# Kernel optimization log

Hardware: AMD Instinct MI355X
Metric: run time of the kernel (lower is better)

The kernel has to match this reference:

```python
import jax, jax.numpy as jnp
import numpy as np

D_MODEL = 1024
D_STATE = 16
D_CONV = 4
EXPAND = 2
D_INNER = EXPAND * D_MODEL          # 2048
DT_RANK = D_INNER // 16             # 128
BATCH = 2
SEQLEN = 1024


def _silu(x):
    return x * jax.nn.sigmoid(x)


def setup_inputs() -> dict:
    key = jax.random.key(0)
    ks = jax.random.split(key, 8)
    s = 0.02
    A_init = jnp.tile(jnp.arange(1, D_STATE + 1, dtype=jnp.float32)[None, :], (D_INNER, 1))
    return {
        "x": jax.random.normal(ks[0], (BATCH, SEQLEN, D_MODEL), jnp.float32),
        "W_in": jax.random.normal(ks[1], (D_MODEL, 2 * D_INNER), jnp.float32) * s,
        "conv_k": jax.random.normal(ks[2], (D_CONV, 1, D_INNER), jnp.float32) * s,  # (kw, in/groups, out)
        "conv_b": jnp.zeros((D_INNER,), jnp.float32),
        "W_xproj": jax.random.normal(ks[3], (D_INNER, DT_RANK + 2 * D_STATE), jnp.float32) * s,
        "W_dt": jax.random.normal(ks[4], (DT_RANK, D_INNER), jnp.float32) * s,
        "b_dt": jnp.zeros((D_INNER,), jnp.float32),
        "A_log": jnp.log(A_init),
        "D": jnp.ones((D_INNER,), jnp.float32),
        "W_out": jax.random.normal(ks[5], (D_INNER, D_MODEL), jnp.float32) * s,
    }


def reference(x, W_in, conv_k, conv_b, W_xproj, W_dt, b_dt, A_log, D, W_out):
    # in_proj and gate split
    xz = x @ W_in                                   # (B, L, 2*Di)
    x_in, z = jnp.split(xz, 2, axis=-1)             # each (B, L, Di)

    # depthwise causal conv1d: left-pad by d_conv-1 (keras padding='causal')
    xp = jnp.pad(x_in, ((0, 0), (D_CONV - 1, 0), (0, 0)))
    x_in = jax.lax.conv_general_dilated(
        xp, conv_k, window_strides=(1,), padding='VALID',
        dimension_numbers=('NWC', 'WIO', 'NWC'),
        feature_group_count=D_INNER) + conv_b
    u = _silu(x_in)                                 # (B, L, Di)

    # input-dependent SSM params
    x_dbl = u @ W_xproj                             # (B, L, dt_rank + 2*N)
    dt_low, Bm, Cm = jnp.split(x_dbl, [DT_RANK, DT_RANK + D_STATE], axis=-1)
    dt = jax.nn.softplus(dt_low @ W_dt + b_dt)      # (B, L, Di)
    A = -jnp.exp(A_log)                             # (Di, N)
    dA = jnp.exp(jnp.einsum('bld,dn->bldn', dt, A)) # (B, L, Di, N)
    dB = jnp.einsum('bld,bln->bldn', dt, Bm)        # (B, L, Di, N)

    # selective scan over sequence length
    def step(h, e):
        a_t, b_t, u_t, c_t = e                      # (B,Di,N), (B,Di,N), (B,Di), (B,N)
        h = a_t * h + b_t * u_t[..., None]
        y_t = jnp.einsum('bdn,bn->bd', h, c_t)
        return h, y_t

    h0 = jnp.zeros((x.shape[0], D_INNER, D_STATE), dtype=x.dtype)
    xs = (jnp.swapaxes(dA, 0, 1), jnp.swapaxes(dB, 0, 1),
          jnp.swapaxes(u, 0, 1), jnp.swapaxes(Cm, 0, 1))
    _, yT = jax.lax.scan(step, h0, xs)              # (L, B, Di)
    y = jnp.swapaxes(yT, 0, 1) + u * D              # skip connection

    return (y * _silu(z)) @ W_out                   # (B, L, d_model)
```

## Files before the change

kernel.cpp:

```cpp
#include <hip/hip_runtime.h>
#include <hip/hip_bf16.h>

#define D_MODEL 1024
#define D_STATE 16
#define D_CONV 4
#define D_INNER 2048
#define DT_RANK 128
#define BATCH 2
#define SEQLEN 1024
#define XCOLS 160
#define NCHUNK 64
#define LCHUNK 16

typedef __hip_bfloat16 bf16;
typedef __attribute__((ext_vector_type(8))) short short8;
typedef __attribute__((ext_vector_type(4))) float f32x4;

__device__ __forceinline__ unsigned short f2bf_bits(float f) {
    bf16 h = __float2bfloat16(f);
    return *(unsigned short*)&h;
}
__device__ __forceinline__ float bfbits_to_f(unsigned int us) {
    return __uint_as_float(us << 16);
}

__device__ __forceinline__ float softplus_f(float x) {
    return fmaxf(x, 0.f) + __logf(1.f + __expf(-fabsf(x)));
}

__device__ __forceinline__ void load16_lds(void* lds, const void* g) {
    __builtin_amdgcn_global_load_lds(
        (const __attribute__((address_space(1))) unsigned int*)g,
        (__attribute__((address_space(3))) unsigned int*)lds, 16, 0, 0);
}

__device__ __forceinline__ void transpose_tile(const float* __restrict__ B,
                                               bf16* __restrict__ Bt,
                                               int K, int N, int nt, int kt,
                                               float (*t)[33], int tid)
{
    const int tx = tid & 31, ty = tid >> 5;
    const int n0 = nt * 32, k0 = kt * 32;
    #pragma unroll
    for (int r = 0; r < 4; ++r) {
        int n = n0 + tx;
        t[ty + r * 8][tx] = (n < N) ? B[(size_t)(k0 + ty + r * 8) * N + n] : 0.f;
    }
    __syncthreads();
    #pragma unroll
    for (int r = 0; r < 4; ++r)
        Bt[(size_t)(n0 + ty + r * 8) * K + k0 + tx] = __float2bfloat16(t[tx][ty + r * 8]);
}

__global__ __launch_bounds__(256)
void prep_kernel(const float* __restrict__ x, bf16* __restrict__ x_bf,
                 const float* __restrict__ W_in, bf16* __restrict__ Win_t,
                 const float* __restrict__ W_xproj, bf16* __restrict__ Wxp_t,
                 const float* __restrict__ W_dt, bf16* __restrict__ Wdt_t,
                 const float* __restrict__ W_out, bf16* __restrict__ Wout_t,
                 const float* __restrict__ A_log, float* __restrict__ Aneg)
{
    __shared__ float t[32][33];
    const int tid = threadIdx.x;
    int blk = blockIdx.x;
    if (blk < 4096) {
        transpose_tile(W_in, Win_t, D_MODEL, 2 * D_INNER, blk & 127, blk >> 7, t, tid);
        return;
    }
    blk -= 4096;
    if (blk < 512) {
        transpose_tile(W_xproj, Wxp_t, D_INNER, XCOLS, blk & 7, blk >> 3, t, tid);
        return;
    }
    blk -= 512;
    if (blk < 256) {
        transpose_tile(W_dt, Wdt_t, DT_RANK, D_INNER, blk & 63, blk >> 6, t, tid);
        return;
    }
    blk -= 256;
    if (blk < 2048) {
        transpose_tile(W_out, Wout_t, D_INNER, D_MODEL, blk & 31, blk >> 5, t, tid);
        return;
    }
    blk -= 2048;
    if (blk < 2048) {
        int i = blk * 256 + tid;
        float4 v = ((const float4*)x)[i];
        ushort4 p;
        p.x = f2bf_bits(v.x); p.y = f2bf_bits(v.y);
        p.z = f2bf_bits(v.z); p.w = f2bf_bits(v.w);
        ((ushort4*)x_bf)[i] = p;
        return;
    }
    blk -= 2048;
    {
        int i = blk * 256 + tid;
        Aneg[i] = -__expf(A_log[i]);
    }
}

template<int BN, int EPI>
__global__ __launch_bounds__(256)
void gemm_mfma(const bf16* __restrict__ A, const bf16* __restrict__ Bt,
               float* __restrict__ C, bf16* __restrict__ Cb,
               const float* __restrict__ bias,
               int M, int N, int K, int ldc, int kchunk)
{
    constexpr int WN = (BN == 128) ? 64 : 32;
    constexpr int NJ = WN / 16;
    __shared__ short As[128 * 32];
    __shared__ short Bs[BN * 32];
    const int tid = threadIdx.x;
    const int lane = tid & 63, wave = tid >> 6;
    const int wm = (wave >> 1) * 64, wn = (wave & 1) * WN;
    const int row0 = blockIdx.y * 128, col0 = blockIdx.x * BN;
    const int r_m = lane & 15, r_q = lane >> 4;
    const int kstart = blockIdx.z * kchunk;
    float* Cz = (EPI == 3) ? C : C + (size_t)blockIdx.z * M * ldc;

    const int srow = tid >> 2, schk = (tid & 3) * 8;
    const bf16* Ag0 = A  + (size_t)(row0 + srow)      * K + kstart + schk;
    const bf16* Ag1 = A  + (size_t)(row0 + srow + 64) * K + kstart + schk;
    const bf16* Bg0 = Bt + (size_t)(col0 + srow)      * K + kstart + schk;
    const bf16* Bg1 = Bt + (size_t)(col0 + srow + 64) * K + kstart + schk;
    short* AsW0 = &As[8 * tid];
    short* AsW1 = &As[8 * tid + 2048];
    short* BsW0 = &Bs[8 * tid];
    short* BsW1 = &Bs[8 * tid + 2048];

    f32x4 acc[4][NJ];
    #pragma unroll
    for (int i = 0; i < 4; ++i)
        #pragma unroll
        for (int j = 0; j < NJ; ++j)
            #pragma unroll
            for (int r = 0; r < 4; ++r) acc[i][j][r] = 0.f;

    for (int k0 = 0; k0 < kchunk; k0 += 32) {
        __syncthreads();
        load16_lds(AsW0, Ag0 + k0);
        load16_lds(AsW1, Ag1 + k0);
        load16_lds(BsW0, Bg0 + k0);
        if (BN == 128) load16_lds(BsW1, Bg1 + k0);
        __syncthreads();
        short8 af[4], bfr[NJ];
        #pragma unroll
        for (int i = 0; i < 4; ++i)
            af[i] = *(const short8*)&As[(wm + i * 16 + r_m) * 32 + r_q * 8];
        #pragma unroll
        for (int j = 0; j < NJ; ++j)
            bfr[j] = *(const short8*)&Bs[(wn + j * 16 + r_m) * 32 + r_q * 8];
        #pragma unroll
        for (int i = 0; i < 4; ++i)
            #pragma unroll
            for (int j = 0; j < NJ; ++j)
                acc[i][j] = __builtin_amdgcn_mfma_f32_16x16x32_bf16(
                    af[i], bfr[j], acc[i][j], 0, 0, 0);
    }

    #pragma unroll
    for (int i = 0; i < 4; ++i) {
        #pragma unroll
        for (int j = 0; j < NJ; ++j) {
            int row = row0 + wm + i * 16 + r_q * 4;
            int col = col0 + wn + j * 16 + r_m;
            if (col < N) {
                if (EPI == 1) {
                    float bv = bias[col];
                    #pragma unroll
                    for (int r = 0; r < 4; ++r)
                        Cb[(size_t)(row + r) * ldc + col] =
                            __float2bfloat16(softplus_f(acc[i][j][r] + bv));
                } else if (EPI == 2) {
                    if (col < D_INNER) {
                        #pragma unroll
                        for (int r = 0; r < 4; ++r)
                            Cz[(size_t)(row + r) * D_INNER + col] = acc[i][j][r];
                    } else {
                        #pragma unroll
                        for (int r = 0; r < 4; ++r)
                            Cb[(size_t)(row + r) * D_INNER + (col - D_INNER)] =
                                __float2bfloat16(acc[i][j][r]);
                    }
                } else if (EPI == 3) {
                    #pragma unroll
                    for (int r = 0; r < 4; ++r)
                        atomicAdd(&Cz[(size_t)(row + r) * ldc + col], acc[i][j][r]);
                } else {
                    #pragma unroll
                    for (int r = 0; r < 4; ++r)
                        Cz[(size_t)(row + r) * ldc + col] = acc[i][j][r];
                }
            }
        }
    }
}

__global__ __launch_bounds__(256)
void reduce_xdbl(const float* __restrict__ Cpart, float* __restrict__ x_dbl,
                 bf16* __restrict__ dtA_bf)
{
    int i = blockIdx.x * 256 + threadIdx.x;
    if (i >= 2048 * XCOLS) return;
    int r = i / XCOLS, c = i - r * XCOLS;
    float s = 0.f;
    #pragma unroll
    for (int z = 0; z < 8; ++z)
        s += Cpart[(size_t)z * 2048 * 256 + (size_t)r * 256 + c];
    x_dbl[i] = s;
    if (c < DT_RANK) dtA_bf[(size_t)r * DT_RANK + c] = __float2bfloat16(s);
}

__global__ __launch_bounds__(256)
void conv_silu_kernel(const float* __restrict__ xz32,
                      const float* __restrict__ conv_k,
                      const float* __restrict__ conv_b,
                      bf16* __restrict__ u_bf)
{
    int idx4 = blockIdx.x * 256 + threadIdx.x;
    int d4 = idx4 & (D_INNER / 4 - 1);
    int t = (idx4 >> 9) & (SEQLEN - 1);
    int b = idx4 >> 19;
    float4 acc = ((const float4*)conv_b)[d4];
    #pragma unroll
    for (int k = 0; k < D_CONV; ++k) {
        int tt = t + k - (D_CONV - 1);
        if (tt >= 0) {
            float4 xv = ((const float4*)xz32)[(size_t)(b * SEQLEN + tt) * (D_INNER / 4) + d4];
            float4 kv = ((const float4*)conv_k)[k * (D_INNER / 4) + d4];
            acc.x = fmaf(xv.x, kv.x, acc.x);
            acc.y = fmaf(xv.y, kv.y, acc.y);
            acc.z = fmaf(xv.z, kv.z, acc.z);
            acc.w = fmaf(xv.w, kv.w, acc.w);
        }
    }
    ushort4 pk;
    pk.x = f2bf_bits(acc.x / (1.f + __expf(-acc.x)));
    pk.y = f2bf_bits(acc.y / (1.f + __expf(-acc.y)));
    pk.z = f2bf_bits(acc.z / (1.f + __expf(-acc.z)));
    pk.w = f2bf_bits(acc.w / (1.f + __expf(-acc.w)));
    ((ushort4*)u_bf)[idx4] = pk;
}

__global__ __launch_bounds__(256)
void scan_phase1(const bf16* __restrict__ dt_sb,
                 const float* __restrict__ Aneg,
                 const bf16* __restrict__ u_bf,
                 const float* __restrict__ x_dbl,
                 unsigned int* __restrict__ PSp)
{
    __shared__ float Bsm[LCHUNK][16];
    const int d = blockIdx.x * 256 + threadIdx.x;
    const int c = blockIdx.y, b = blockIdx.z;
    const int t0 = c * LCHUNK;
    {
        int tt = threadIdx.x >> 4, n = threadIdx.x & 15;
        Bsm[tt][n] = x_dbl[(size_t)(b * SEQLEN + t0 + tt) * XCOLS + DT_RANK + n];
    }
    float A_row[D_STATE];
    {
        const float4* a4 = (const float4*)(Aneg + d * D_STATE);
        #pragma unroll
        for (int q = 0; q < 4; ++q) {
            float4 v = a4[q];
            A_row[q*4+0]=v.x; A_row[q*4+1]=v.y; A_row[q*4+2]=v.z; A_row[q*4+3]=v.w;
        }
    }
    __syncthreads();
    float P[D_STATE], S[D_STATE];
    #pragma unroll
    for (int n = 0; n < D_STATE; ++n) { P[n] = 1.f; S[n] = 0.f; }
    const bf16* dpp = dt_sb + (size_t)(b * SEQLEN + t0) * D_INNER + d;
    const bf16* upp = u_bf + (size_t)(b * SEQLEN + t0) * D_INNER + d;
    #pragma unroll
    for (int t = 0; t < LCHUNK; ++t) {
        float dtv = __bfloat162float(dpp[(size_t)t * D_INNER]);
        float du = dtv * __bfloat162float(upp[(size_t)t * D_INNER]);
        const float4* b4 = (const float4*)&Bsm[t][0];
        #pragma unroll
        for (int q = 0; q < 4; ++q) {
            float4 v = b4[q];
            float Bn[4] = {v.x, v.y, v.z, v.w};
            #pragma unroll
            for (int e = 0; e < 4; ++e) {
                int n = q * 4 + e;
                float a = __expf(dtv * A_row[n]);
                P[n] *= a;
                S[n] = fmaf(a, S[n], du * Bn[e]);
            }
        }
    }
    const size_t base = ((size_t)(b * NCHUNK + c) * D_STATE) * D_INNER + d;
    #pragma unroll
    for (int n = 0; n < D_STATE; ++n)
        PSp[base + (size_t)n * D_INNER] =
            ((unsigned int)f2bf_bits(S[n]) << 16) | f2bf_bits(P[n]);
}

__global__ __launch_bounds__(256)
void scan_phase2(const unsigned int* __restrict__ PSp, bf16* __restrict__ Hin)
{
    const int d = blockIdx.x * 256 + threadIdx.x;
    const int n = blockIdx.y;
    const int b = blockIdx.z;
    float h = 0.f;
    #pragma unroll 8
    for (int c = 0; c < NCHUNK; ++c) {
        const size_t idx = ((size_t)(b * NCHUNK + c) * D_STATE + n) * D_INNER + d;
        unsigned int ps = PSp[idx];
        float Pv = bfbits_to_f(ps & 0xffffu);
        float Sv = bfbits_to_f(ps >> 16);
        Hin[idx] = __float2bfloat16(h);
        h = fmaf(Pv, h, Sv);
    }
}

__global__ __launch_bounds__(256)
void scan_phase3(const bf16* __restrict__ dt_sb,
                 const float* __restrict__ Aneg,
                 const bf16* __restrict__ u_bf,
                 const float* __restrict__ x_dbl,
                 const float* __restrict__ Dvec,
                 const bf16* __restrict__ z_bf,
                 const bf16* __restrict__ Hin,
                 bf16* __restrict__ g_bf)
{
    __shared__ float BCs[LCHUNK][32];
    const int d = blockIdx.x * 256 + threadIdx.x;
    const int c = blockIdx.y, b = blockIdx.z;
    const int t0 = c * LCHUNK;
    {
        int i0 = threadIdx.x;
        int tt = i0 >> 5, col = i0 & 31;
        BCs[tt][col] = x_dbl[(size_t)(b * SEQLEN + t0 + tt) * XCOLS + DT_RANK + col];
        int i1 = i0 + 256;
        tt = i1 >> 5; col = i1 & 31;
        BCs[tt][col] = x_dbl[(size_t)(b * SEQLEN + t0 + tt) * XCOLS + DT_RANK + col];
    }
    float A_row[D_STATE];
    {
        const float4* a4 = (const float4*)(Aneg + d * D_STATE);
        #pragma unroll
        for (int q = 0; q < 4; ++q) {
            float4 v = a4[q];
            A_row[q*4+0]=v.x; A_row[q*4+1]=v.y; A_row[q*4+2]=v.z; A_row[q*4+3]=v.w;
        }
    }
    const float Dd = Dvec[d];
    __syncthreads();
    float h[D_STATE];
    const size_t base = ((size_t)(b * NCHUNK + c) * D_STATE) * D_INNER + d;
    #pragma unroll
    for (int n = 0; n < D_STATE; ++n)
        h[n] = __bfloat162float(Hin[base + (size_t)n * D_INNER]);
    const bf16* dpp = dt_sb + (size_t)(b * SEQLEN + t0) * D_INNER + d;
    const bf16* upp = u_bf + (size_t)(b * SEQLEN + t0) * D_INNER + d;
    const bf16* zpp = z_bf + (size_t)(b * SEQLEN + t0) * D_INNER + d;
    bf16* gpp = g_bf + (size_t)(b * SEQLEN + t0) * D_INNER + d;
    #pragma unroll
    for (int t = 0; t < LCHUNK; ++t) {
        float dtv = __bfloat162float(dpp[(size_t)t * D_INNER]);
        float uv = __bfloat162float(upp[(size_t)t * D_INNER]);
        float du = dtv * uv;
        float y = 0.f;
        const float4* bc4 = (const float4*)&BCs[t][0];
        #pragma unroll
        for (int q = 0; q < 4; ++q) {
            float4 v = bc4[q];
            float4 w = bc4[q + 4];
            float Bn[4] = {v.x, v.y, v.z, v.w};
            float Cn[4] = {w.x, w.y, w.z, w.w};
            #pragma unroll
            for (int e = 0; e < 4; ++e) {
                int n = q * 4 + e;
                float a = __expf(dtv * A_row[n]);
                h[n] = fmaf(a, h[n], du * Bn[e]);
                y = fmaf(h[n], Cn[e], y);
            }
        }
        float zv = __bfloat162float(zpp[(size_t)t * D_INNER]);
        float gy = y + uv * Dd;
        float sz = zv / (1.f + __expf(-zv));
        gpp[(size_t)t * D_INNER] = __float2bfloat16(gy * sz);
    }
}

extern "C" void kernel_launch(void* const* d_in, const int* in_sizes, int n_in,
                              void* d_out, int out_size, void* d_ws, size_t ws_size,
                              hipStream_t stream)
{
    const float* x      = (const float*)d_in[0];
    const float* W_in   = (const float*)d_in[1];
    const float* conv_k = (const float*)d_in[2];
    const float* conv_b = (const float*)d_in[3];
    const float* W_xproj= (const float*)d_in[4];
    const float* W_dt   = (const float*)d_in[5];
    const float* b_dt   = (const float*)d_in[6];
    const float* A_log  = (const float*)d_in[7];
    const float* Dvec   = (const float*)d_in[8];
    const float* W_out  = (const float*)d_in[9];
    float* out = (float*)d_out;

    const int BL = BATCH * SEQLEN;
    const size_t PS_ELEMS = (size_t)BATCH * NCHUNK * D_STATE * D_INNER;

    float* ws     = (float*)d_ws;
    float* xz32   = ws;
    float* x_dbl  = xz32   + (size_t)BL * D_INNER;
    float* Cpart3 = x_dbl  + (size_t)BL * XCOLS;
    unsigned int* PSp = (unsigned int*)(Cpart3 + 4194304);
    bf16* Hin     = (bf16*)(PSp + PS_ELEMS);
    float* Aneg   = (float*)(Hin + PS_ELEMS);
    bf16*  x_bf   = (bf16*)Cpart3;
    bf16* Win_t  = (bf16*)(Aneg + 32768);
    bf16* u_bf   = Win_t + (size_t)4096 * 1024;
    bf16* Wxp_t  = u_bf  + (size_t)BL * D_INNER;
    bf16* dtA_bf = Wxp_t + (size_t)256 * 2048;
    bf16* Wdt_t  = dtA_bf+ (size_t)BL * DT_RANK;
    bf16* g_bf   = Wdt_t + (size_t)2048 * 128;
    bf16* Wout_t = g_bf  + (size_t)BL * D_INNER;
    bf16* dt_sb  = Wout_t+ (size_t)1024 * 2048;
    bf16* z_bf   = dt_sb + (size_t)BL * D_INNER;

    hipMemsetAsync(out, 0, (size_t)out_size * sizeof(float), stream);
    prep_kernel<<<4096 + 512 + 256 + 2048 + 2048 + 128, 256, 0, stream>>>(
        x, x_bf, W_in, Win_t, W_xproj, Wxp_t, W_dt, Wdt_t, W_out, Wout_t, A_log, Aneg);

    gemm_mfma<128, 2><<<dim3(32, 16, 1), 256, 0, stream>>>(
        x_bf, Win_t, xz32, z_bf, nullptr, BL, 2 * D_INNER, D_MODEL, D_INNER, D_MODEL);

    conv_silu_kernel<<<(BL * D_INNER / 4) / 256, 256, 0, stream>>>(xz32, conv_k, conv_b, u_bf);

    gemm_mfma<64, 0><<<dim3(4, 16, 8), 256, 0, stream>>>(
        u_bf, Wxp_t, Cpart3, nullptr, nullptr, BL, 256, D_INNER, 256, 256);
    reduce_xdbl<<<(BL * XCOLS + 255) / 256, 256, 0, stream>>>(Cpart3, x_dbl, dtA_bf);

    gemm_mfma<64, 1><<<dim3(32, 16, 1), 256, 0, stream>>>(
        dtA_bf, Wdt_t, nullptr, dt_sb, b_dt, BL, D_INNER, DT_RANK, D_INNER, DT_RANK);

    scan_phase1<<<dim3(D_INNER / 256, NCHUNK, BATCH), 256, 0, stream>>>(
        dt_sb, Aneg, u_bf, x_dbl, PSp);
    scan_phase2<<<dim3(D_INNER / 256, D_STATE, BATCH), 256, 0, stream>>>(PSp, Hin);
    scan_phase3<<<dim3(D_INNER / 256, NCHUNK, BATCH), 256, 0, stream>>>(
        dt_sb, Aneg, u_bf, x_dbl, Dvec, z_bf, Hin, g_bf);

    gemm_mfma<64, 3><<<dim3(16, 16, 2), 256, 0, stream>>>(
        g_bf, Wout_t, out, nullptr, nullptr, BL, D_MODEL, D_INNER, D_MODEL, D_MODEL);
}
```

Before: 238.2 us.

## Prescale A by log2e for exp2, fold output zeroing into prep, reuse conv window

Scales A by log2(e) in the prep kernel so the scan phases can call exp2f directly and skip the multiply inside __expf. Replaces the separate hipMemsetAsync of the output with extra zeroing blocks in prep_kernel, removing one operation from the stream. Rewrites conv_silu so each thread produces four consecutive timesteps from a 7-row sliding window, cutting redundant loads of xz32 and conv weights. In exchange the conv kernel launches four times fewer threads and each thread does more work.

```diff
diff --git a/kernel.cpp b/kernel.cpp
--- a/kernel.cpp
+++ b/kernel.cpp
@@ -52,13 +52,16 @@
         Bt[(size_t)(n0 + ty + r * 8) * K + k0 + tx] = __float2bfloat16(t[tx][ty + r * 8]);
 }
 
+#define LOG2E 1.4426950408889634f
+
 __global__ __launch_bounds__(256)
 void prep_kernel(const float* __restrict__ x, bf16* __restrict__ x_bf,
                  const float* __restrict__ W_in, bf16* __restrict__ Win_t,
                  const float* __restrict__ W_xproj, bf16* __restrict__ Wxp_t,
                  const float* __restrict__ W_dt, bf16* __restrict__ Wdt_t,
                  const float* __restrict__ W_out, bf16* __restrict__ Wout_t,
-                 const float* __restrict__ A_log, float* __restrict__ Aneg)
+                 const float* __restrict__ A_log, float* __restrict__ A2,
+                 float* __restrict__ out_zero)
 {
     __shared__ float t[32][33];
     const int tid = threadIdx.x;
@@ -93,9 +96,16 @@
         return;
     }
     blk -= 2048;
+    if (blk < 128) {
+        int i = blk * 256 + tid;
+        A2[i] = -__expf(A_log[i]) * LOG2E;
+        return;
+    }
+    blk -= 128;
     {
         int i = blk * 256 + tid;
-        Aneg[i] = -__expf(A_log[i]);
+        float4 z = {0.f, 0.f, 0.f, 0.f};
+        ((float4*)out_zero)[i] = z;
     }
 }
 
@@ -217,34 +227,48 @@
                       const float* __restrict__ conv_b,
                       bf16* __restrict__ u_bf)
 {
-    int idx4 = blockIdx.x * 256 + threadIdx.x;
-    int d4 = idx4 & (D_INNER / 4 - 1);
-    int t = (idx4 >> 9) & (SEQLEN - 1);
-    int b = idx4 >> 19;
-    float4 acc = ((const float4*)conv_b)[d4];
-    #pragma unroll
-    for (int k = 0; k < D_CONV; ++k) {
-        int tt = t + k - (D_CONV - 1);
-        if (tt >= 0) {
-            float4 xv = ((const float4*)xz32)[(size_t)(b * SEQLEN + tt) * (D_INNER / 4) + d4];
-            float4 kv = ((const float4*)conv_k)[k * (D_INNER / 4) + d4];
-            acc.x = fmaf(xv.x, kv.x, acc.x);
-            acc.y = fmaf(xv.y, kv.y, acc.y);
-            acc.z = fmaf(xv.z, kv.z, acc.z);
-            acc.w = fmaf(xv.w, kv.w, acc.w);
-        }
-    }
-    ushort4 pk;
-    pk.x = f2bf_bits(acc.x / (1.f + __expf(-acc.x)));
-    pk.y = f2bf_bits(acc.y / (1.f + __expf(-acc.y)));
-    pk.z = f2bf_bits(acc.z / (1.f + __expf(-acc.z)));
-    pk.w = f2bf_bits(acc.w / (1.f + __expf(-acc.w)));
-    ((ushort4*)u_bf)[idx4] = pk;
+    int idx = blockIdx.x * 256 + threadIdx.x;
+    int d4 = idx & (D_INNER / 4 - 1);
+    int t4 = (idx >> 9) & (SEQLEN / 4 - 1);
+    int b  = idx >> 17;
+    const int t0 = t4 * 4;
+    float4 kv[D_CONV];
+    #pragma unroll
+    for (int k = 0; k < D_CONV; ++k)
+        kv[k] = ((const float4*)conv_k)[k * (D_INNER / 4) + d4];
+    const float4 bias = ((const float4*)conv_b)[d4];
+    float4 xv[7];
+    #pragma unroll
+    for (int j = 0; j < 7; ++j) {
+        int tt = t0 - 3 + j;
+        if (tt >= 0)
+            xv[j] = ((const float4*)xz32)[(size_t)(b * SEQLEN + tt) * (D_INNER / 4) + d4];
+        else
+            xv[j] = make_float4(0.f, 0.f, 0.f, 0.f);
+    }
+    #pragma unroll
+    for (int i = 0; i < 4; ++i) {
+        float4 acc = bias;
+        #pragma unroll
+        for (int k = 0; k < D_CONV; ++k) {
+            float4 xvk = xv[i + k];
+            acc.x = fmaf(xvk.x, kv[k].x, acc.x);
+            acc.y = fmaf(xvk.y, kv[k].y, acc.y);
+            acc.z = fmaf(xvk.z, kv[k].z, acc.z);
+            acc.w = fmaf(xvk.w, kv[k].w, acc.w);
+        }
+        ushort4 pk;
+        pk.x = f2bf_bits(acc.x / (1.f + __expf(-acc.x)));
+        pk.y = f2bf_bits(acc.y / (1.f + __expf(-acc.y)));
+        pk.z = f2bf_bits(acc.z / (1.f + __expf(-acc.z)));
+        pk.w = f2bf_bits(acc.w / (1.f + __expf(-acc.w)));
+        ((ushort4*)u_bf)[(size_t)(b * SEQLEN + t0 + i) * (D_INNER / 4) + d4] = pk;
+    }
 }
 
 __global__ __launch_bounds__(256)
 void scan_phase1(const bf16* __restrict__ dt_sb,
-                 const float* __restrict__ Aneg,
+                 const float* __restrict__ A2,
                  const bf16* __restrict__ u_bf,
                  const float* __restrict__ x_dbl,
                  unsigned int* __restrict__ PSp)
@@ -259,7 +283,7 @@
     }
     float A_row[D_STATE];
     {
-        const float4* a4 = (const float4*)(Aneg + d * D_STATE);
+        const float4* a4 = (const float4*)(A2 + d * D_STATE);
         #pragma unroll
         for (int q = 0; q < 4; ++q) {
             float4 v = a4[q];
@@ -284,7 +308,7 @@
             #pragma unroll
             for (int e = 0; e < 4; ++e) {
                 int n = q * 4 + e;
-                float a = __expf(dtv * A_row[n]);
+                float a = exp2f(dtv * A_row[n]);
                 P[n] *= a;
                 S[n] = fmaf(a, S[n], du * Bn[e]);
             }
@@ -317,7 +341,7 @@
 
 __global__ __launch_bounds__(256)
 void scan_phase3(const bf16* __restrict__ dt_sb,
-                 const float* __restrict__ Aneg,
+                 const float* __restrict__ A2,
                  const bf16* __restrict__ u_bf,
                  const float* __restrict__ x_dbl,
                  const float* __restrict__ Dvec,
@@ -339,7 +363,7 @@
     }
     float A_row[D_STATE];
     {
-        const float4* a4 = (const float4*)(Aneg + d * D_STATE);
+        const float4* a4 = (const float4*)(A2 + d * D_STATE);
         #pragma unroll
         for (int q = 0; q < 4; ++q) {
             float4 v = a4[q];
@@ -373,7 +397,7 @@
             #pragma unroll
             for (int e = 0; e < 4; ++e) {
                 int n = q * 4 + e;
-                float a = __expf(dtv * A_row[n]);
+                float a = exp2f(dtv * A_row[n]);
                 h[n] = fmaf(a, h[n], du * Bn[e]);
                 y = fmaf(h[n], Cn[e], y);
             }
@@ -410,9 +434,9 @@
     float* Cpart3 = x_dbl  + (size_t)BL * XCOLS;
     unsigned int* PSp = (unsigned int*)(Cpart3 + 4194304);
     bf16* Hin     = (bf16*)(PSp + PS_ELEMS);
-    float* Aneg   = (float*)(Hin + PS_ELEMS);
+    float* A2v    = (float*)(Hin + PS_ELEMS);
     bf16*  x_bf   = (bf16*)Cpart3;
-    bf16* Win_t  = (bf16*)(Aneg + 32768);
+    bf16* Win_t  = (bf16*)(A2v + 32768);
     bf16* u_bf   = Win_t + (size_t)4096 * 1024;
     bf16* Wxp_t  = u_bf  + (size_t)BL * D_INNER;
     bf16* dtA_bf = Wxp_t + (size_t)256 * 2048;
@@ -422,14 +446,15 @@
     bf16* dt_sb  = Wout_t+ (size_t)1024 * 2048;
     bf16* z_bf   = dt_sb + (size_t)BL * D_INNER;
 
-    hipMemsetAsync(out, 0, (size_t)out_size * sizeof(float), stream);
-    prep_kernel<<<4096 + 512 + 256 + 2048 + 2048 + 128, 256, 0, stream>>>(
-        x, x_bf, W_in, Win_t, W_xproj, Wxp_t, W_dt, Wdt_t, W_out, Wout_t, A_log, Aneg);
+    prep_kernel<<<4096 + 512 + 256 + 2048 + 2048 + 128 + 2048, 256, 0, stream>>>(
+        x, x_bf, W_in, Win_t, W_xproj, Wxp_t, W_dt, Wdt_t, W_out, Wout_t,
+        A_log, A2v, out);
 
     gemm_mfma<128, 2><<<dim3(32, 16, 1), 256, 0, stream>>>(
         x_bf, Win_t, xz32, z_bf, nullptr, BL, 2 * D_INNER, D_MODEL, D_INNER, D_MODEL);
 
-    conv_silu_kernel<<<(BL * D_INNER / 4) / 256, 256, 0, stream>>>(xz32, conv_k, conv_b, u_bf);
+    conv_silu_kernel<<<(BL * D_INNER / 16) / 256, 256, 0, stream>>>(
+        xz32, conv_k, conv_b, u_bf);
 
     gemm_mfma<64, 0><<<dim3(4, 16, 8), 256, 0, stream>>>(
         u_bf, Wxp_t, Cpart3, nullptr, nullptr, BL, 256, D_INNER, 256, 256);
@@ -439,10 +464,10 @@
         dtA_bf, Wdt_t, nullptr, dt_sb, b_dt, BL, D_INNER, DT_RANK, D_INNER, DT_RANK);
 
     scan_phase1<<<dim3(D_INNER / 256, NCHUNK, BATCH), 256, 0, stream>>>(
-        dt_sb, Aneg, u_bf, x_dbl, PSp);
+        dt_sb, A2v, u_bf, x_dbl, PSp);
     scan_phase2<<<dim3(D_INNER / 256, D_STATE, BATCH), 256, 0, stream>>>(PSp, Hin);
     scan_phase3<<<dim3(D_INNER / 256, NCHUNK, BATCH), 256, 0, stream>>>(
-        dt_sb, Aneg, u_bf, x_dbl, Dvec, z_bf, Hin, g_bf);
+        dt_sb, A2v, u_bf, x_dbl, Dvec, z_bf, Hin, g_bf);
 
     gemm_mfma<64, 3><<<dim3(16, 16, 2), 256, 0, stream>>>(
         g_bf, Wout_t, out, nullptr, nullptr, BL, D_MODEL, D_INNER, D_MODEL, D_MODEL);
```

New measurement: 242.6 us. About the same (+1.8%).
